# Kernel tuning notes

Hardware: AMD Instinct MI355X
Metric: run time of the kernel (lower is better)

## Reference

```python
import jax, jax.numpy as jnp
import numpy as np

B, S, HID, NH = 2, 2048, 2048, 16
ROPE, NOPE, VDIM = 64, 64, 128
QHEAD = ROPE + NOPE            # 128
QLORA = HID // 3               # 682
KVLORA = HID // 8              # 256
THETA = 128000.0
SCALE = 1.0 / np.sqrt(QHEAD)   # deepseek softmax_scale = q_head_dim**-0.5
EPS = 1e-6


def rmsnorm(x, w):
    var = jnp.mean(x.astype(jnp.float32) ** 2, axis=-1, keepdims=True)
    return (x.astype(jnp.float32) * jax.lax.rsqrt(var + EPS)).astype(x.dtype) * w


def rope_cos_sin(seq, dim, theta):
    inv = 1.0 / (theta ** (jnp.arange(0, dim, 2, dtype=jnp.float32) / dim))
    t = jnp.arange(seq, dtype=jnp.float32)
    freqs = jnp.outer(t, inv)                      # [S, dim/2]
    emb = jnp.concatenate([freqs, freqs], axis=-1)  # [S, dim]
    return jnp.cos(emb), jnp.sin(emb)


def apply_rope(x, cos, sin):
    # deepseek interleave: view(b,h,s,d/2,2).transpose(-1,-2).reshape, then rotate_half rope
    b, h, s, d = x.shape
    x = x.reshape(b, h, s, d // 2, 2).transpose(0, 1, 2, 4, 3).reshape(b, h, s, d)
    x1, x2 = jnp.split(x, 2, axis=-1)
    rot = jnp.concatenate([-x2, x1], axis=-1)
    return x * cos + rot * sin


def setup_inputs() -> dict:
    key = jax.random.key(0)
    ks = jax.random.split(key, 8)
    s = lambda fan_in: 1.0 / np.sqrt(fan_in)
    return {
        "x":        jax.random.normal(ks[0], (B, S, HID), jnp.float32),
        "q_a_w":    jax.random.normal(ks[1], (HID, QLORA), jnp.float32) * s(HID),
        "q_a_ln_w": jnp.ones((QLORA,), jnp.float32),
        "q_b_w":    jax.random.normal(ks[2], (QLORA, NH * QHEAD), jnp.float32) * s(QLORA),
        "kv_a_w":   jax.random.normal(ks[3], (HID, KVLORA + ROPE), jnp.float32) * s(HID),
        "kv_a_ln_w": jnp.ones((KVLORA,), jnp.float32),
        "kv_b_w":   jax.random.normal(ks[4], (KVLORA, NH * (NOPE + VDIM)), jnp.float32) * s(KVLORA),
        "o_w":      jax.random.normal(ks[5], (NH * VDIM, HID), jnp.float32) * s(NH * VDIM),
    }


def reference(x, q_a_w, q_a_ln_w, q_b_w, kv_a_w, kv_a_ln_w, kv_b_w, o_w):
    b, s, _ = x.shape
    # Q: low-rank down-proj -> RMSNorm -> up-proj
    q = rmsnorm(x @ q_a_w, q_a_ln_w) @ q_b_w               # [b,s,NH*QHEAD]
    q = q.reshape(b, s, NH, QHEAD).transpose(0, 2, 1, 3)   # [b,NH,s,QHEAD]
    q_nope, q_pe = q[..., :NOPE], q[..., NOPE:]
    # KV: compressed latent + shared rope key
    ckv_kpe = x @ kv_a_w                                   # [b,s,KVLORA+ROPE]
    ckv, k_pe = ckv_kpe[..., :KVLORA], ckv_kpe[..., KVLORA:]
    k_pe = k_pe.reshape(b, 1, s, ROPE)                     # shared across heads
    kv = rmsnorm(ckv, kv_a_ln_w) @ kv_b_w                  # [b,s,NH*(NOPE+VDIM)]
    kv = kv.reshape(b, s, NH, NOPE + VDIM).transpose(0, 2, 1, 3)
    k_nope, v = kv[..., :NOPE], kv[..., NOPE:]             # [b,NH,s,NOPE], [b,NH,s,VDIM]
    # decoupled RoPE on the rope split only
    cos, sin = rope_cos_sin(s, ROPE, THETA)
    q_pe = apply_rope(q_pe, cos, sin)
    k_pe = apply_rope(k_pe, cos, sin)
    qf = jnp.concatenate([q_nope, q_pe], axis=-1)          # [b,NH,s,QHEAD]
    kf = jnp.concatenate([k_nope, jnp.broadcast_to(k_pe, (b, NH, s, ROPE))], axis=-1)
    scores = jnp.einsum('bhqd,bhkd->bhqk', qf, kf) * SCALE
    causal = jnp.tril(jnp.ones((s, s), bool))
    scores = jnp.where(causal, scores, jnp.float32(-1e9))
    attn = jax.nn.softmax(scores.astype(jnp.float32), axis=-1).astype(qf.dtype)
    out = jnp.einsum('bhqk,bhkd->bhqd', attn, v)           # [b,NH,s,VDIM]
    out = out.transpose(0, 2, 1, 3).reshape(b, s, NH * VDIM)
    return out @ o_w                                       # [b,s,HID]
```

## Files before the change

### kernel.cpp

```cpp
#include <hip/hip_runtime.h>
#include <hip/hip_bf16.h>

typedef __attribute__((ext_vector_type(8))) short short8;
typedef __attribute__((ext_vector_type(4))) float f32x4;

using bf16 = __hip_bfloat16;

static constexpr int B_ = 2, S_ = 2048, HID_ = 2048, NH_ = 16;
static constexpr int ROPE_ = 64, VDIM_ = 128, QHEAD_ = 128;
static constexpr int QLORA_ = 682, KVLORA_ = 256;
static constexpr int QLORA_P = 704;
static constexpr int NQA_P = 768;
static constexpr int NKVA_P = 384;
static constexpr int NA_ = NQA_P + NKVA_P;
static constexpr float THETA_ = 128000.0f;
static constexpr float SCALE_ = 0.08838834764831845f;
static constexpr float SCL2_ = 0.08838834764831845f * 1.4426950408889634f;
static constexpr float EPS_ = 1e-6f;
static constexpr int BS_ = B_ * S_;

__device__ __forceinline__ void gl2lds16(const void* g, void* l) {
    __builtin_amdgcn_global_load_lds(
        (const __attribute__((address_space(1))) unsigned int*)g,
        (__attribute__((address_space(3))) unsigned int*)l, 16, 0, 0);
}

struct bf16x4_s { bf16 x, y, z, w; };

struct TD { const float* src; bf16* dst; int Ksrc, Nsrc, Kpad, tilesX, off, perm; };
struct TDs { TD d[5]; };
static constexpr int PREP_TILES = 8576;

__global__ void k_prep(TDs P, const float* __restrict__ x, bf16* __restrict__ xb,
                       float* __restrict__ ct, float* __restrict__ st) {
    __shared__ float tile[32][33];
    if (blockIdx.x >= PREP_TILES) {
        int bid = blockIdx.x - PREP_TILES;
        int t = threadIdx.y * 32 + threadIdx.x;
        if (bid < 8192) {
            int i = bid * 256 + t;
            float4 v = reinterpret_cast<const float4*>(x)[i];
            bf16x4_s o;
            o.x = __float2bfloat16(v.x); o.y = __float2bfloat16(v.y);
            o.z = __float2bfloat16(v.z); o.w = __float2bfloat16(v.w);
            reinterpret_cast<bf16x4_s*>(xb)[i] = o;
        } else {
            int idx = (bid - 8192) * 256 + t;
            int tpos = idx >> 5, j = idx & 31;
            float inv = expf(-(float)j * (logf(THETA_) / 32.0f));
            float f = (float)tpos * inv;
            ct[idx] = cosf(f);
            st[idx] = sinf(f);
        }
        return;
    }
    int flat = blockIdx.x;
    int di = 0;
    #pragma unroll
    for (int i = 1; i < 5; ++i) if (flat >= P.d[i].off) di = i;
    TD d = P.d[di];
    int local = flat - d.off;
    int xt = local % d.tilesX, yt = local / d.tilesX;
    int kb = xt * 32, nb = yt * 32;
    int tx = threadIdx.x, ty = threadIdx.y;
    #pragma unroll
    for (int i = 0; i < 32; i += 8) {
        int k = kb + ty + i, n = nb + tx;
        tile[ty + i][tx] = (k < d.Ksrc && n < d.Nsrc) ? d.src[(size_t)k * d.Nsrc + n] : 0.0f;
    }
    __syncthreads();
    #pragma unroll
    for (int i = 0; i < 32; i += 8) {
        int n = nb + ty + i, k = kb + tx;
        int nd = n;
        if (d.perm) {
            int h = n / 192, dd = n - h * 192;
            nd = (dd < 64) ? h * 64 + dd : 1024 + h * 128 + (dd - 64);
        }
        d.dst[(size_t)nd * d.Kpad + k] = __float2bfloat16(tile[tx][ty + i]);
    }
}

#define GEMM_VARS                                                                        \
    __shared__ bf16 As[128 * 64];                                                        \
    __shared__ bf16 Bs[128 * 64];                                                        \
    const int t = threadIdx.x;                                                           \
    const int lane = t & 63, w = t >> 6;                                                 \
    const int l15 = lane & 15, l4 = lane >> 4;                                           \
    const int wr = (w >> 1) * 64, wc = (w & 1) * 64;

#define GEMM_CORE(Aptr, Bptr, LDA, LDB, KDIM, M0V, N0V)                                  \
    const int m0 = (M0V), n0 = (N0V);                                                    \
    f32x4 acc[4][4] = {};                                                                \
    for (int k0 = 0; k0 < (KDIM); k0 += 64) {                                            \
        _Pragma("unroll")                                                                \
        for (int i = 0; i < 4; ++i) {                                                    \
            int cid = t + i * 256;                                                       \
            int row = cid >> 3;                                                          \
            int ch = (cid & 7) ^ (row & 7);                                              \
            gl2lds16((Aptr) + (size_t)(m0 + row) * (LDA) + k0 + ch * 8,                  \
                     reinterpret_cast<char*>(As) + cid * 16);                            \
            gl2lds16((Bptr) + (size_t)(n0 + row) * (LDB) + k0 + ch * 8,                  \
                     reinterpret_cast<char*>(Bs) + cid * 16);                            \
        }                                                                                \
        __syncthreads();                                                                 \
        _Pragma("unroll")                                                                \
        for (int kk = 0; kk < 2; ++kk) {                                                 \
            short8 a[4], b[4];                                                           \
            _Pragma("unroll")                                                            \
            for (int m = 0; m < 4; ++m) {                                                \
                int row = wr + m * 16 + l15;                                             \
                int ch = (kk * 4 + l4) ^ (row & 7);                                      \
                a[m] = *reinterpret_cast<const short8*>(                                 \
                    reinterpret_cast<const char*>(As) + row * 128 + ch * 16);            \
            }                                                                            \
            _Pragma("unroll")                                                            \
            for (int n = 0; n < 4; ++n) {                                                \
                int row = wc + n * 16 + l15;                                             \
                int ch = (kk * 4 + l4) ^ (row & 7);                                      \
                b[n] = *reinterpret_cast<const short8*>(                                 \
                    reinterpret_cast<const char*>(Bs) + row * 128 + ch * 16);            \
            }                                                                            \
            _Pragma("unroll")                                                            \
            for (int m = 0; m < 4; ++m)                                                  \
                _Pragma("unroll")                                                        \
                for (int n = 0; n < 4; ++n)                                              \
                    acc[m][n] = __builtin_amdgcn_mfma_f32_16x16x32_bf16(a[m], b[n],      \
                                                                       acc[m][n], 0, 0, 0); \
        }                                                                                \
        __syncthreads();                                                                 \
    }

template <typename OutT>
__launch_bounds__(256)
__global__ void gemm_bt(const bf16* __restrict__ A, const bf16* __restrict__ Bt,
                        OutT* __restrict__ C, int K, int lda, int ldb, int ldc)
{
    GEMM_VARS
    GEMM_CORE(A, Bt, lda, ldb, K, blockIdx.y * 128, blockIdx.x * 128)
    #pragma unroll
    for (int m = 0; m < 4; ++m)
        #pragma unroll
        for (int n = 0; n < 4; ++n)
            #pragma unroll
            for (int j = 0; j < 4; ++j) {
                int r = m0 + wr + m * 16 + l4 * 4 + j;
                int c = n0 + wc + n * 16 + l15;
                float v = acc[m][n][j];
                if constexpr (sizeof(OutT) == 2) C[(size_t)r * ldc + c] = __float2bfloat16(v);
                else                             C[(size_t)r * ldc + c] = v;
            }
}

__launch_bounds__(256)
__global__ void gemm_up(const bf16* __restrict__ qan, const bf16* __restrict__ qb_wt,
                        const float* __restrict__ ct, const float* __restrict__ st,
                        bf16* __restrict__ Qf,
                        const bf16* __restrict__ ckvn, const bf16* __restrict__ kvb_wt,
                        bf16* __restrict__ knope, bf16* __restrict__ Vt)
{
    GEMM_VARS
    if (blockIdx.x < 16) {
        GEMM_CORE(qan, qb_wt, QLORA_P, QLORA_P, QLORA_P, blockIdx.y * 128, blockIdx.x * 128)
        (void)n0;
        const int h = blockIdx.x;
        if (wc == 0) {
            #pragma unroll
            for (int m = 0; m < 4; ++m)
                #pragma unroll
                for (int n = 0; n < 4; ++n)
                    #pragma unroll
                    for (int j = 0; j < 4; ++j) {
                        int r = m0 + wr + m * 16 + l4 * 4 + j;
                        int c = n * 16 + l15;
                        int s = r & (S_ - 1), bq = r >> 11;
                        Qf[((size_t)(bq * NH_ + h) * S_ + s) * 128 + c] =
                            __float2bfloat16(acc[m][n][j] * SCL2_);
                    }
        } else {
            #pragma unroll
            for (int m = 0; m < 4; ++m)
                #pragma unroll
                for (int n = 0; n < 4; ++n)
                    #pragma unroll
                    for (int j = 0; j < 4; ++j) {
                        int r = m0 + wr + m * 16 + l4 * 4 + j;
                        int p = n * 16 + l15;
                        int jj = p >> 1, odd = p & 1;
                        float v = acc[m][n][j];
                        float pr = __shfl_xor(v, 1);
                        float e0 = odd ? pr : v, e1 = odd ? v : pr;
                        int s = r & (S_ - 1), bq = r >> 11;
                        float c_ = ct[s * 32 + jj], s_ = st[s * 32 + jj];
                        float ov = odd ? (e1 * c_ + e0 * s_) : (e0 * c_ - e1 * s_);
                        int c_out = 64 + (odd ? 32 : 0) + jj;
                        Qf[((size_t)(bq * NH_ + h) * S_ + s) * 128 + c_out] =
                            __float2bfloat16(ov * SCL2_);
                    }
        }
    } else {
        GEMM_CORE(ckvn, kvb_wt, KVLORA_, KVLORA_, KVLORA_, blockIdx.y * 128,
                  (blockIdx.x - 16) * 128)
        if (n0 < 1024) {
            #pragma unroll
            for (int m = 0; m < 4; ++m)
                #pragma unroll
                for (int n = 0; n < 4; ++n)
                    #pragma unroll
                    for (int j = 0; j < 4; ++j) {
                        int r = m0 + wr + m * 16 + l4 * 4 + j;
                        int c = n0 + wc + n * 16 + l15;
                        knope[(size_t)r * 1024 + c] = __float2bfloat16(acc[m][n][j]);
                    }
        } else {
            const int h = (n0 - 1024) >> 7;
            const int bq = m0 >> 11;
            const int bh = bq * NH_ + h;
            #pragma unroll
            for (int m = 0; m < 4; ++m)
                #pragma unroll
                for (int n = 0; n < 4; ++n) {
                    int cl = wc + n * 16 + l15;
                    int rb = m0 + wr + m * 16 + l4 * 4;
                    int s = rb & (S_ - 1);
                    ushort4 pk;
                    {
                        bf16 h0 = __float2bfloat16(acc[m][n][0]);
                        bf16 h1 = __float2bfloat16(acc[m][n][1]);
                        bf16 h2 = __float2bfloat16(acc[m][n][2]);
                        bf16 h3 = __float2bfloat16(acc[m][n][3]);
                        pk.x = *reinterpret_cast<unsigned short*>(&h0);
                        pk.y = *reinterpret_cast<unsigned short*>(&h1);
                        pk.z = *reinterpret_cast<unsigned short*>(&h2);
                        pk.w = *reinterpret_cast<unsigned short*>(&h3);
                    }
                    *reinterpret_cast<ushort4*>(Vt + ((size_t)bh * 128 + cl) * S_ + s) = pk;
                }
        }
    }
}

__launch_bounds__(256)
__global__ void k_rms_rope(const bf16* __restrict__ qac,
                           const float* __restrict__ qln, const float* __restrict__ kvln,
                           const float* __restrict__ ct, const float* __restrict__ st,
                           bf16* __restrict__ qan, bf16* __restrict__ ckvn, bf16* __restrict__ kr)
{
    __shared__ float red[8];
    int bs = blockIdx.x;
    int t = threadIdx.x, lane = t & 63, w = t >> 6;
    int s = bs & (S_ - 1);
    const bf16* qrow = qac + (size_t)bs * NA_;
    const bf16* crow = qrow + NQA_P;
    float sq = 0.f, sk;
    for (int c = t; c < QLORA_; c += 256) { float v = __bfloat162float(qrow[c]); sq += v * v; }
    { float v = __bfloat162float(crow[t]); sk = v * v; }
    #pragma unroll
    for (int m = 1; m < 64; m <<= 1) { sq += __shfl_xor(sq, m); sk += __shfl_xor(sk, m); }
    if (lane == 0) { red[w] = sq; red[4 + w] = sk; }
    __syncthreads();
    sq = red[0] + red[1] + red[2] + red[3];
    sk = red[4] + red[5] + red[6] + red[7];
    float qs = rsqrtf(sq / (float)QLORA_ + EPS_);
    float ks = rsqrtf(sk / (float)KVLORA_ + EPS_);
    for (int c = t; c < QLORA_P; c += 256)
        qan[(size_t)bs * QLORA_P + c] =
            (c < QLORA_) ? __float2bfloat16(__bfloat162float(qrow[c]) * qs * qln[c])
                         : __float2bfloat16(0.0f);
    ckvn[(size_t)bs * KVLORA_ + t] = __float2bfloat16(__bfloat162float(crow[t]) * ks * kvln[t]);
    if (t < 64) {
        int j = t & 31;
        float c_ = ct[s * 32 + j], s_ = st[s * 32 + j];
        float e0 = __bfloat162float(crow[KVLORA_ + 2 * j]);
        float e1 = __bfloat162float(crow[KVLORA_ + 2 * j + 1]);
        float v = (t < 32) ? (e0 * c_ - e1 * s_) : (e1 * c_ + e0 * s_);
        kr[(size_t)bs * 64 + t] = __float2bfloat16(v);
    }
}

__launch_bounds__(512, 4)
__global__ void k_flash(const bf16* __restrict__ Qf, const bf16* __restrict__ knope,
                        const bf16* __restrict__ kr, const bf16* __restrict__ Vt,
                        bf16* __restrict__ attn_out)
{
    __shared__ bf16 Ks[2][64 * 128];
    __shared__ bf16 Vs[2][128 * 64];
    __shared__ bf16 Ps[8][16 * 64];

    const int t = threadIdx.x, lane = t & 63, w = t >> 6;
    const int l15 = lane & 15, l4 = lane >> 4;
    const int qb = (blockIdx.y < 8) ? (15 - blockIdx.y) : (blockIdx.y - 8);
    const int bh = blockIdx.x;
    const int q0 = qb * 128;
    const int b = bh >> 4, h = bh & 15;
    const int r0 = q0 + w * 16;

    short8 qa_[4];
    {
        const bf16* qrow = Qf + ((size_t)bh * S_ + r0 + l15) * 128;
        #pragma unroll
        for (int kk = 0; kk < 4; ++kk)
            qa_[kk] = *reinterpret_cast<const short8*>(qrow + kk * 32 + l4 * 8);
    }

    const bf16 *kSrc0, *kSrc1, *vSrc0, *vSrc1;
    size_t kStp0, kStp1;
    {
        int cid = t, row = cid >> 4, ch = (cid & 15) ^ (row & 7);
        kSrc0 = (ch < 8) ? knope + (size_t)(b * S_ + row) * 1024 + h * 64 + ch * 8
                         : kr + (size_t)(b * S_ + row) * 64 + (ch - 8) * 8;
        kStp0 = (ch < 8) ? (size_t)64 * 1024 : (size_t)64 * 64;
    }
    {
        int cid = t + 512, row = cid >> 4, ch = (cid & 15) ^ (row & 7);
        kSrc1 = (ch < 8) ? knope + (size_t)(b * S_ + row) * 1024 + h * 64 + ch * 8
                         : kr + (size_t)(b * S_ + row) * 64 + (ch - 8) * 8;
        kStp1 = (ch < 8) ? (size_t)64 * 1024 : (size_t)64 * 64;
    }
    {
        const bf16* Vg = Vt + (size_t)bh * 128 * S_;
        int cid = t, row = cid >> 3, ch = (cid & 7) ^ (row & 7);
        vSrc0 = Vg + (size_t)row * S_ + ch * 8;
        cid = t + 512; row = cid >> 3; ch = (cid & 7) ^ (row & 7);
        vSrc1 = Vg + (size_t)row * S_ + ch * 8;
    }
    auto stage = [&](int buf) {
        gl2lds16(kSrc0, reinterpret_cast<char*>(Ks[buf]) + t * 16);
        gl2lds16(kSrc1, reinterpret_cast<char*>(Ks[buf]) + (t + 512) * 16);
        gl2lds16(vSrc0, reinterpret_cast<char*>(Vs[buf]) + t * 16);
        gl2lds16(vSrc1, reinterpret_cast<char*>(Vs[buf]) + (t + 512) * 16);
        kSrc0 += kStp0; kSrc1 += kStp1; vSrc0 += 64; vSrc1 += 64;
    };

    const int NT = qb * 2 + 2;
    stage(0);
    __syncthreads();

    f32x4 o[8] = {};
    float m_r = -1e30f, l_r = 0.f;

    int cur = 0;
    for (int kb = 0; kb < NT; ++kb) {
        const int k0 = kb * 64;
        if (kb + 1 < NT) stage(cur ^ 1);

        if (k0 <= r0 + 15) {
            f32x4 sfr[4] = {};
            __builtin_amdgcn_s_setprio(1);
            #pragma unroll
            for (int kk = 0; kk < 4; ++kk) {
                short8 kf[4];
                #pragma unroll
                for (int m = 0; m < 4; ++m) {
                    int row = m * 16 + l15;
                    int ch = (kk * 4 + l4) ^ (row & 7);
                    kf[m] = *reinterpret_cast<const short8*>(
                        reinterpret_cast<const char*>(Ks[cur]) + row * 256 + ch * 16);
                }
                #pragma unroll
                for (int m = 0; m < 4; ++m)
                    sfr[m] = __builtin_amdgcn_mfma_f32_16x16x32_bf16(kf[m], qa_[kk], sfr[m], 0, 0, 0);
            }
            __builtin_amdgcn_s_setprio(0);

            const int qrow = r0 + l15;
            if (k0 + 63 > r0) {
                #pragma unroll
                for (int m = 0; m < 4; ++m) {
                    int kbase = k0 + m * 16 + l4 * 4;
                    #pragma unroll
                    for (int j = 0; j < 4; ++j)
                        if (kbase + j > qrow) sfr[m][j] = -1e30f;
                }
            }

            float rm;
            {
                float a0 = fmaxf(fmaxf(sfr[0][0], sfr[0][1]), fmaxf(sfr[0][2], sfr[0][3]));
                float a1 = fmaxf(fmaxf(sfr[1][0], sfr[1][1]), fmaxf(sfr[1][2], sfr[1][3]));
                float a2 = fmaxf(fmaxf(sfr[2][0], sfr[2][1]), fmaxf(sfr[2][2], sfr[2][3]));
                float a3 = fmaxf(fmaxf(sfr[3][0], sfr[3][1]), fmaxf(sfr[3][2], sfr[3][3]));
                rm = fmaxf(fmaxf(a0, a1), fmaxf(a2, a3));
            }
            rm = fmaxf(rm, __shfl_xor(rm, 16));
            rm = fmaxf(rm, __shfl_xor(rm, 32));

            if (__ballot(rm > m_r + 8.0f)) {
                float mn = fmaxf(m_r, rm);
                float alpha = exp2f(m_r - mn);
                m_r = mn;
                l_r *= alpha;
                float aj[4];
                #pragma unroll
                for (int j = 0; j < 4; ++j) aj[j] = __shfl(alpha, l4 * 4 + j);
                #pragma unroll
                for (int n = 0; n < 8; ++n)
                    #pragma unroll
                    for (int j = 0; j < 4; ++j) o[n][j] *= aj[j];
            }

            char* pb = reinterpret_cast<char*>(Ps[w]);
            float rs = 0.f;
            #pragma unroll
            for (int m = 0; m < 4; ++m) {
                float p0 = exp2f(sfr[m][0] - m_r);
                float p1 = exp2f(sfr[m][1] - m_r);
                float p2 = exp2f(sfr[m][2] - m_r);
                float p3 = exp2f(sfr[m][3] - m_r);
                rs += (p0 + p1) + (p2 + p3);
                union { __hip_bfloat162 h; unsigned int u; } cl, ch2;
                cl.h  = __float22bfloat162_rn(make_float2(p0, p1));
                ch2.h = __float22bfloat162_rn(make_float2(p2, p3));
                int kloc = m * 16 + l4 * 4;
                int chnk = (kloc >> 3) ^ (l15 & 7);
                uint2 pk2; pk2.x = cl.u; pk2.y = ch2.u;
                *reinterpret_cast<uint2*>(pb + l15 * 128 + chnk * 16 + (kloc & 7) * 2) = pk2;
            }
            rs += __shfl_xor(rs, 16);
            rs += __shfl_xor(rs, 32);
            l_r += rs;

            __builtin_amdgcn_s_setprio(1);
            #pragma unroll
            for (int kk = 0; kk < 2; ++kk) {
                int pch = (kk * 4 + l4) ^ (l15 & 7);
                short8 pa = *reinterpret_cast<const short8*>(pb + l15 * 128 + pch * 16);
                #pragma unroll
                for (int n = 0; n < 8; ++n) {
                    int row = n * 16 + l15;
                    int ch = (kk * 4 + l4) ^ (row & 7);
                    short8 vb = *reinterpret_cast<const short8*>(
                        reinterpret_cast<const char*>(Vs[cur]) + row * 128 + ch * 16);
                    o[n] = __builtin_amdgcn_mfma_f32_16x16x32_bf16(pa, vb, o[n], 0, 0, 0);
                }
            }
            __builtin_amdgcn_s_setprio(0);
        }
        __syncthreads();
        cur ^= 1;
    }

    float lj[4];
    #pragma unroll
    for (int j = 0; j < 4; ++j) lj[j] = __shfl(l_r, l4 * 4 + j);
    size_t obase = ((size_t)(b * S_) + q0 + w * 16) * (size_t)(NH_ * VDIM_) + h * VDIM_;
    #pragma unroll
    for (int n = 0; n < 8; ++n)
        #pragma unroll
        for (int j = 0; j < 4; ++j) {
            int r = l4 * 4 + j;
            int c = n * 16 + l15;
            attn_out[obase + (size_t)r * (NH_ * VDIM_) + c] = __float2bfloat16(o[n][j] / lj[j]);
        }
}

extern "C" void kernel_launch(void* const* d_in, const int* in_sizes, int n_in,
                              void* d_out, int out_size, void* d_ws, size_t ws_size,
                              hipStream_t stream)
{
    (void)in_sizes; (void)n_in; (void)out_size;
    const float* x       = (const float*)d_in[0];
    const float* q_a_w   = (const float*)d_in[1];
    const float* q_a_ln  = (const float*)d_in[2];
    const float* q_b_w   = (const float*)d_in[3];
    const float* kv_a_w  = (const float*)d_in[4];
    const float* kv_a_ln = (const float*)d_in[5];
    const float* kv_b_w  = (const float*)d_in[6];
    const float* o_w     = (const float*)d_in[7];
    float* out = (float*)d_out;

    char* ws = (char*)d_ws;
    size_t off = 0;
    auto alloc = [&](size_t bytes) -> char* {
        char* p = ws + off;
        off += (bytes + 255) & ~(size_t)255;
        return p;
    };

    bf16* xb     = (bf16*)alloc((size_t)BS_ * HID_ * 2);
    bf16* a_wt   = (bf16*)alloc((size_t)NA_ * HID_ * 2);
    bf16* qb_wt  = (bf16*)alloc((size_t)2048 * QLORA_P * 2);
    bf16* kvb_wt = (bf16*)alloc((size_t)3072 * KVLORA_ * 2);
    bf16* ow_t   = (bf16*)alloc((size_t)2048 * 2048 * 2);
    float* ct    = (float*)alloc((size_t)S_ * 32 * 4);
    float* st    = (float*)alloc((size_t)S_ * 32 * 4);
    bf16* qac    = (bf16*)alloc((size_t)BS_ * NA_ * 2);
    bf16* qan    = (bf16*)alloc((size_t)BS_ * QLORA_P * 2);
    bf16* ckvn   = (bf16*)alloc((size_t)BS_ * KVLORA_ * 2);
    bf16* kr     = (bf16*)alloc((size_t)BS_ * 64 * 2);
    bf16* knope  = (bf16*)alloc((size_t)BS_ * 1024 * 2);
    bf16* Vt     = (bf16*)alloc((size_t)BS_ * 2048 * 2);
    bf16* attn   = (bf16*)alloc((size_t)BS_ * 2048 * 2);

    bf16* Qf = xb;

    if (ws_size < off) return;

    TDs P;
    P.d[0] = TD{ q_a_w,  a_wt,                      2048,  682, 2048, 64,    0, 0 };
    P.d[1] = TD{ kv_a_w, a_wt + (size_t)NQA_P*2048, 2048,  320, 2048, 64, 1536, 0 };
    P.d[2] = TD{ q_b_w,  qb_wt,                      682, 2048,  704, 22, 2304, 0 };
    P.d[3] = TD{ kv_b_w, kvb_wt,                     256, 3072,  256,  8, 3712, 1 };
    P.d[4] = TD{ o_w,    ow_t,                      2048, 2048, 2048, 64, 4480, 0 };
    k_prep<<<PREP_TILES + 8192 + 256, dim3(32, 8), 0, stream>>>(P, x, xb, ct, st);

    gemm_bt<bf16><<<dim3(NA_ / 128, BS_ / 128), 256, 0, stream>>>(xb, a_wt, qac,
                                                                  HID_, HID_, HID_, NA_);

    k_rms_rope<<<BS_, 256, 0, stream>>>(qac, q_a_ln, kv_a_ln, ct, st, qan, ckvn, kr);

    gemm_up<<<dim3(16 + 24, BS_ / 128), 256, 0, stream>>>(qan, qb_wt, ct, st, Qf,
                                                          ckvn, kvb_wt, knope, Vt);

    k_flash<<<dim3(B_ * NH_, S_ / 128), 512, 0, stream>>>(Qf, knope, kr, Vt, attn);

    gemm_bt<float><<<dim3(2048 / 128, BS_ / 128), 256, 0, stream>>>(attn, ow_t, out,
                                                                    HID_, HID_, HID_, 2048);
}
```

Measured before the change: 229.5 us.

## Fold RMSNorm weights into up-projection weights and apply row scales in epilogue

```diff
diff --git a/kernel.cpp b/kernel.cpp
--- a/kernel.cpp
+++ b/kernel.cpp
@@ -27,7 +27,11 @@
 
 struct bf16x4_s { bf16 x, y, z, w; };
 
-struct TD { const float* src; bf16* dst; int Ksrc, Nsrc, Kpad, tilesX, off, perm; };
+__device__ __forceinline__ float bfLo(unsigned int u) { return __uint_as_float(u << 16); }
+__device__ __forceinline__ float bfHi(unsigned int u) { return __uint_as_float(u & 0xffff0000u); }
+
+struct TD { const float* src; bf16* dst; const float* colw;
+            int Ksrc, Nsrc, Kpad, tilesX, off, perm; };
 struct TDs { TD d[5]; };
 static constexpr int PREP_TILES = 8576;
 
@@ -66,18 +70,28 @@
     #pragma unroll
     for (int i = 0; i < 32; i += 8) {
         int k = kb + ty + i, n = nb + tx;
-        tile[ty + i][tx] = (k < d.Ksrc && n < d.Nsrc) ? d.src[(size_t)k * d.Nsrc + n] : 0.0f;
+        float v = (k < d.Ksrc && n < d.Nsrc) ? d.src[(size_t)k * d.Nsrc + n] : 0.0f;
+        if (d.colw && k < d.Ksrc) v *= d.colw[k];
+        tile[ty + i][tx] = v;
     }
     __syncthreads();
-    #pragma unroll
-    for (int i = 0; i < 32; i += 8) {
-        int n = nb + ty + i, k = kb + tx;
+    int u = ty * 32 + tx;
+    int kp = u & 15;
+    int nl = u >> 4;
+    #pragma unroll
+    for (int half = 0; half < 2; ++half) {
+        int n_loc = nl + 16 * half;
+        int n = nb + n_loc;
         int nd = n;
         if (d.perm) {
             int h = n / 192, dd = n - h * 192;
             nd = (dd < 64) ? h * 64 + dd : 1024 + h * 128 + (dd - 64);
         }
-        d.dst[(size_t)nd * d.Kpad + k] = __float2bfloat16(tile[tx][ty + i]);
+        bf16 lo = __float2bfloat16(tile[2 * kp][n_loc]);
+        bf16 hi = __float2bfloat16(tile[2 * kp + 1][n_loc]);
+        unsigned int pk = (unsigned int)*reinterpret_cast<unsigned short*>(&lo) |
+                          ((unsigned int)*reinterpret_cast<unsigned short*>(&hi) << 16);
+        *reinterpret_cast<unsigned int*>(d.dst + (size_t)nd * d.Kpad + kb + 2 * kp) = pk;
     }
 }
 
@@ -153,38 +167,47 @@
 }
 
 __launch_bounds__(256)
-__global__ void gemm_up(const bf16* __restrict__ qan, const bf16* __restrict__ qb_wt,
+__global__ void gemm_up(const bf16* __restrict__ qac, const bf16* __restrict__ qb_wt,
                         const float* __restrict__ ct, const float* __restrict__ st,
-                        bf16* __restrict__ Qf,
-                        const bf16* __restrict__ ckvn, const bf16* __restrict__ kvb_wt,
+                        const float* __restrict__ qs, bf16* __restrict__ Qf,
+                        const bf16* __restrict__ kvb_wt, const float* __restrict__ ks,
                         bf16* __restrict__ knope, bf16* __restrict__ Vt)
 {
     GEMM_VARS
     if (blockIdx.x < 16) {
-        GEMM_CORE(qan, qb_wt, QLORA_P, QLORA_P, QLORA_P, blockIdx.y * 128, blockIdx.x * 128)
+        GEMM_CORE(qac, qb_wt, NA_, QLORA_P, QLORA_P, blockIdx.y * 128, blockIdx.x * 128)
         (void)n0;
         const int h = blockIdx.x;
         if (wc == 0) {
             #pragma unroll
-            for (int m = 0; m < 4; ++m)
+            for (int m = 0; m < 4; ++m) {
+                int rb = m0 + wr + m * 16 + l4 * 4;
+                float q4[4];
+                #pragma unroll
+                for (int j = 0; j < 4; ++j) q4[j] = qs[rb + j] * SCL2_;
                 #pragma unroll
                 for (int n = 0; n < 4; ++n)
                     #pragma unroll
                     for (int j = 0; j < 4; ++j) {
-                        int r = m0 + wr + m * 16 + l4 * 4 + j;
+                        int r = rb + j;
                         int c = n * 16 + l15;
                         int s = r & (S_ - 1), bq = r >> 11;
                         Qf[((size_t)(bq * NH_ + h) * S_ + s) * 128 + c] =
-                            __float2bfloat16(acc[m][n][j] * SCL2_);
+                            __float2bfloat16(acc[m][n][j] * q4[j]);
                     }
+            }
         } else {
             #pragma unroll
-            for (int m = 0; m < 4; ++m)
+            for (int m = 0; m < 4; ++m) {
+                int rb = m0 + wr + m * 16 + l4 * 4;
+                float q4[4];
+                #pragma unroll
+                for (int j = 0; j < 4; ++j) q4[j] = qs[rb + j] * SCL2_;
                 #pragma unroll
                 for (int n = 0; n < 4; ++n)
                     #pragma unroll
                     for (int j = 0; j < 4; ++j) {
-                        int r = m0 + wr + m * 16 + l4 * 4 + j;
+                        int r = rb + j;
                         int p = n * 16 + l15;
                         int jj = p >> 1, odd = p & 1;
                         float v = acc[m][n][j];
@@ -195,40 +218,49 @@
                         float ov = odd ? (e1 * c_ + e0 * s_) : (e0 * c_ - e1 * s_);
                         int c_out = 64 + (odd ? 32 : 0) + jj;
                         Qf[((size_t)(bq * NH_ + h) * S_ + s) * 128 + c_out] =
-                            __float2bfloat16(ov * SCL2_);
+                            __float2bfloat16(ov * q4[j]);
                     }
+            }
         }
     } else {
-        GEMM_CORE(ckvn, kvb_wt, KVLORA_, KVLORA_, KVLORA_, blockIdx.y * 128,
+        GEMM_CORE(qac + NQA_P, kvb_wt, NA_, KVLORA_, KVLORA_, blockIdx.y * 128,
                   (blockIdx.x - 16) * 128)
         if (n0 < 1024) {
             #pragma unroll
-            for (int m = 0; m < 4; ++m)
+            for (int m = 0; m < 4; ++m) {
+                int rb = m0 + wr + m * 16 + l4 * 4;
+                float k4[4];
+                #pragma unroll
+                for (int j = 0; j < 4; ++j) k4[j] = ks[rb + j];
                 #pragma unroll
                 for (int n = 0; n < 4; ++n)
                     #pragma unroll
                     for (int j = 0; j < 4; ++j) {
-                        int r = m0 + wr + m * 16 + l4 * 4 + j;
                         int c = n0 + wc + n * 16 + l15;
-                        knope[(size_t)r * 1024 + c] = __float2bfloat16(acc[m][n][j]);
+                        knope[(size_t)(rb + j) * 1024 + c] =
+                            __float2bfloat16(acc[m][n][j] * k4[j]);
                     }
+            }
         } else {
             const int h = (n0 - 1024) >> 7;
             const int bq = m0 >> 11;
             const int bh = bq * NH_ + h;
             #pragma unroll
-            for (int m = 0; m < 4; ++m)
+            for (int m = 0; m < 4; ++m) {
+                int rb = m0 + wr + m * 16 + l4 * 4;
+                int s = rb & (S_ - 1);
+                float k4[4];
+                #pragma unroll
+                for (int j = 0; j < 4; ++j) k4[j] = ks[rb + j];
                 #pragma unroll
                 for (int n = 0; n < 4; ++n) {
                     int cl = wc + n * 16 + l15;
-                    int rb = m0 + wr + m * 16 + l4 * 4;
-                    int s = rb & (S_ - 1);
                     ushort4 pk;
                     {
-                        bf16 h0 = __float2bfloat16(acc[m][n][0]);
-                        bf16 h1 = __float2bfloat16(acc[m][n][1]);
-                        bf16 h2 = __float2bfloat16(acc[m][n][2]);
-                        bf16 h3 = __float2bfloat16(acc[m][n][3]);
+                        bf16 h0 = __float2bfloat16(acc[m][n][0] * k4[0]);
+                        bf16 h1 = __float2bfloat16(acc[m][n][1] * k4[1]);
+                        bf16 h2 = __float2bfloat16(acc[m][n][2] * k4[2]);
+                        bf16 h3 = __float2bfloat16(acc[m][n][3] * k4[3]);
                         pk.x = *reinterpret_cast<unsigned short*>(&h0);
                         pk.y = *reinterpret_cast<unsigned short*>(&h1);
                         pk.z = *reinterpret_cast<unsigned short*>(&h2);
@@ -236,43 +268,48 @@
                     }
                     *reinterpret_cast<ushort4*>(Vt + ((size_t)bh * 128 + cl) * S_ + s) = pk;
                 }
+            }
         }
     }
 }
 
 __launch_bounds__(256)
-__global__ void k_rms_rope(const bf16* __restrict__ qac,
-                           const float* __restrict__ qln, const float* __restrict__ kvln,
-                           const float* __restrict__ ct, const float* __restrict__ st,
-                           bf16* __restrict__ qan, bf16* __restrict__ ckvn, bf16* __restrict__ kr)
+__global__ void k_scales(const bf16* __restrict__ qac,
+                         const float* __restrict__ ct, const float* __restrict__ st,
+                         float* __restrict__ qs, float* __restrict__ ks,
+                         bf16* __restrict__ kr)
 {
     __shared__ float red[8];
     int bs = blockIdx.x;
     int t = threadIdx.x, lane = t & 63, w = t >> 6;
     int s = bs & (S_ - 1);
-    const bf16* qrow = qac + (size_t)bs * NA_;
-    const bf16* crow = qrow + NQA_P;
-    float sq = 0.f, sk;
-    for (int c = t; c < QLORA_; c += 256) { float v = __bfloat162float(qrow[c]); sq += v * v; }
-    { float v = __bfloat162float(crow[t]); sk = v * v; }
+    const unsigned int* qp = reinterpret_cast<const unsigned int*>(qac + (size_t)bs * NA_);
+    float sq = 0.f, sk = 0.f;
+    for (int p = t; p < 341; p += 256) {
+        unsigned int u = qp[p];
+        float a = bfLo(u), b = bfHi(u);
+        sq += a * a + b * b;
+    }
+    if (t < 128) {
+        unsigned int u = qp[384 + t];
+        float a = bfLo(u), b = bfHi(u);
+        sk = a * a + b * b;
+    }
     #pragma unroll
     for (int m = 1; m < 64; m <<= 1) { sq += __shfl_xor(sq, m); sk += __shfl_xor(sk, m); }
     if (lane == 0) { red[w] = sq; red[4 + w] = sk; }
     __syncthreads();
-    sq = red[0] + red[1] + red[2] + red[3];
-    sk = red[4] + red[5] + red[6] + red[7];
-    float qs = rsqrtf(sq / (float)QLORA_ + EPS_);
-    float ks = rsqrtf(sk / (float)KVLORA_ + EPS_);
-    for (int c = t; c < QLORA_P; c += 256)
-        qan[(size_t)bs * QLORA_P + c] =
-            (c < QLORA_) ? __float2bfloat16(__bfloat162float(qrow[c]) * qs * qln[c])
-                         : __float2bfloat16(0.0f);
-    ckvn[(size_t)bs * KVLORA_ + t] = __float2bfloat16(__bfloat162float(crow[t]) * ks * kvln[t]);
+    if (t == 0) {
+        sq = red[0] + red[1] + red[2] + red[3];
+        sk = red[4] + red[5] + red[6] + red[7];
+        qs[bs] = rsqrtf(sq / (float)QLORA_ + EPS_);
+        ks[bs] = rsqrtf(sk / (float)KVLORA_ + EPS_);
+    }
     if (t < 64) {
         int j = t & 31;
         float c_ = ct[s * 32 + j], s_ = st[s * 32 + j];
-        float e0 = __bfloat162float(crow[KVLORA_ + 2 * j]);
-        float e1 = __bfloat162float(crow[KVLORA_ + 2 * j + 1]);
+        unsigned int u = qp[512 + j];
+        float e0 = bfLo(u), e1 = bfHi(u);
         float v = (t < 32) ? (e0 * c_ - e1 * s_) : (e1 * c_ + e0 * s_);
         kr[(size_t)bs * 64 + t] = __float2bfloat16(v);
     }
@@ -440,9 +477,9 @@
         cur ^= 1;
     }
 
-    float lj[4];
-    #pragma unroll
-    for (int j = 0; j < 4; ++j) lj[j] = __shfl(l_r, l4 * 4 + j);
+    float rj[4];
+    #pragma unroll
+    for (int j = 0; j < 4; ++j) rj[j] = __builtin_amdgcn_rcpf(__shfl(l_r, l4 * 4 + j));
     size_t obase = ((size_t)(b * S_) + q0 + w * 16) * (size_t)(NH_ * VDIM_) + h * VDIM_;
     #pragma unroll
     for (int n = 0; n < 8; ++n)
@@ -450,7 +487,7 @@
         for (int j = 0; j < 4; ++j) {
             int r = l4 * 4 + j;
             int c = n * 16 + l15;
-            attn_out[obase + (size_t)r * (NH_ * VDIM_) + c] = __float2bfloat16(o[n][j] / lj[j]);
+            attn_out[obase + (size_t)r * (NH_ * VDIM_) + c] = __float2bfloat16(o[n][j] * rj[j]);
         }
 }
 
@@ -485,8 +522,8 @@
     float* ct    = (float*)alloc((size_t)S_ * 32 * 4);
     float* st    = (float*)alloc((size_t)S_ * 32 * 4);
     bf16* qac    = (bf16*)alloc((size_t)BS_ * NA_ * 2);
-    bf16* qan    = (bf16*)alloc((size_t)BS_ * QLORA_P * 2);
-    bf16* ckvn   = (bf16*)alloc((size_t)BS_ * KVLORA_ * 2);
+    float* qs    = (float*)alloc((size_t)BS_ * 4);
+    float* ksc   = (float*)alloc((size_t)BS_ * 4);
     bf16* kr     = (bf16*)alloc((size_t)BS_ * 64 * 2);
     bf16* knope  = (bf16*)alloc((size_t)BS_ * 1024 * 2);
     bf16* Vt     = (bf16*)alloc((size_t)BS_ * 2048 * 2);
@@ -497,20 +534,20 @@
     if (ws_size < off) return;
 
     TDs P;
-    P.d[0] = TD{ q_a_w,  a_wt,                      2048,  682, 2048, 64,    0, 0 };
-    P.d[1] = TD{ kv_a_w, a_wt + (size_t)NQA_P*2048, 2048,  320, 2048, 64, 1536, 0 };
-    P.d[2] = TD{ q_b_w,  qb_wt,                      682, 2048,  704, 22, 2304, 0 };
-    P.d[3] = TD{ kv_b_w, kvb_wt,                     256, 3072,  256,  8, 3712, 1 };
-    P.d[4] = TD{ o_w,    ow_t,                      2048, 2048, 2048, 64, 4480, 0 };
+    P.d[0] = TD{ q_a_w,  a_wt,                     nullptr, 2048,  682, 2048, 64,    0, 0 };
+    P.d[1] = TD{ kv_a_w, a_wt + (size_t)NQA_P*2048,nullptr, 2048,  320, 2048, 64, 1536, 0 };
+    P.d[2] = TD{ q_b_w,  qb_wt,                    q_a_ln,   682, 2048,  704, 22, 2304, 0 };
+    P.d[3] = TD{ kv_b_w, kvb_wt,                   kv_a_ln,  256, 3072,  256,  8, 3712, 1 };
+    P.d[4] = TD{ o_w,    ow_t,                     nullptr, 2048, 2048, 2048, 64, 4480, 0 };
     k_prep<<<PREP_TILES + 8192 + 256, dim3(32, 8), 0, stream>>>(P, x, xb, ct, st);
 
     gemm_bt<bf16><<<dim3(NA_ / 128, BS_ / 128), 256, 0, stream>>>(xb, a_wt, qac,
                                                                   HID_, HID_, HID_, NA_);
 
-    k_rms_rope<<<BS_, 256, 0, stream>>>(qac, q_a_ln, kv_a_ln, ct, st, qan, ckvn, kr);
-
-    gemm_up<<<dim3(16 + 24, BS_ / 128), 256, 0, stream>>>(qan, qb_wt, ct, st, Qf,
-                                                          ckvn, kvb_wt, knope, Vt);
+    k_scales<<<BS_, 256, 0, stream>>>(qac, ct, st, qs, ksc, kr);
+
+    gemm_up<<<dim3(16 + 24, BS_ / 128), 256, 0, stream>>>(qac, qb_wt, ct, st, qs, Qf,
+                                                          kvb_wt, ksc, knope, Vt);
 
     k_flash<<<dim3(B_ * NH_, S_ / 128), 512, 0, stream>>>(Qf, knope, kr, Vt, attn);
 
```

Result: no change. 225.4 us (-1.8%).
